# Kernel tuning notes

Measured on AMD Instinct MI355X. Metric: run time of the kernel, lower is better.

## Reference

```python
import jax, jax.numpy as jnp
import numpy as np

N = 50000        # nodes
E = 800000       # edges
FEAT = 64        # cfg.feature_dim
HID = 128        # cfg.hidden_dim
G = 8            # num graphs
EPS = 1e-5       # LayerNorm eps
MIN_DEPTH, MAX_DEPTH = 0.1, 3.0


def _ln(x, g, b):
    m = jnp.mean(x, axis=-1, keepdims=True)
    v = jnp.mean((x - m) ** 2, axis=-1, keepdims=True)
    return (x - m) * jax.lax.rsqrt(v + EPS) * g + b


def setup_inputs() -> dict:
    key = jax.random.key(0)
    ks = jax.random.split(key, 32)
    f32 = jnp.float32
    inp = {}
    inp['x'] = jax.random.normal(ks[0], (N, FEAT), dtype=f32)
    inp['edge_index'] = jax.random.randint(ks[1], (2, E), 0, N)
    inp['batch'] = jnp.sort(jax.random.randint(ks[2], (N,), 0, G))
    # input_projection: Linear(FEAT,HID) + LayerNorm
    inp['in_w'] = jax.random.normal(ks[3], (FEAT, HID), dtype=f32) * (1.0 / np.sqrt(FEAT))
    inp['in_b'] = jnp.zeros((HID,), f32)
    inp['in_ln_g'] = jnp.ones((HID,), f32)
    inp['in_ln_b'] = jnp.zeros((HID,), f32)
    # epigenetics
    inp['methylation'] = jnp.zeros((HID,), f32)
    inp['histones'] = jnp.zeros((4,), f32)
    inp['log_depth'] = jnp.zeros((), f32)
    # NeuralODEFunc: 3 stacked GCNConv(HID,HID) + LayerNorms, gate MLP, residual scalar
    inp['gcn_w'] = jax.random.normal(ks[4], (3, HID, HID), dtype=f32) * (1.0 / np.sqrt(HID))
    inp['gcn_b'] = jnp.zeros((3, HID), f32)
    inp['ln_g'] = jnp.ones((3, HID), f32)
    inp['ln_b'] = jnp.zeros((3, HID), f32)
    inp['gate_w'] = jax.random.normal(ks[5], (2 * HID, HID), dtype=f32) * (1.0 / np.sqrt(2 * HID))
    inp['gate_b'] = jnp.zeros((HID,), f32)
    inp['residual_weight'] = jnp.asarray(0.1, f32)
    # output_projection: Linear(HID,HID) + LayerNorm
    inp['out_w'] = jax.random.normal(ks[6], (HID, HID), dtype=f32) * (1.0 / np.sqrt(HID))
    inp['out_b'] = jnp.zeros((HID,), f32)
    inp['out_ln_g'] = jnp.ones((HID,), f32)
    inp['out_ln_b'] = jnp.zeros((HID,), f32)
    return inp


def reference(x, edge_index, batch, in_w, in_b, in_ln_g, in_ln_b, methylation,
              histones, log_depth, gcn_w, gcn_b, ln_g, ln_b, gate_w, gate_b,
              residual_weight, out_w, out_b, out_ln_g, out_ln_b):
    n = x.shape[0]
    src, dst = edge_index[0], edge_index[1]

    # input_projection (Dropout is identity in eval)
    h = jax.nn.relu(_ln(x @ in_w + in_b, in_ln_g, in_ln_b))

    # epigenetic regulation (chromatin_accessibility goes through .item() -> constant)
    meth_sil = jnp.mean(jax.nn.sigmoid(methylation))
    hm = jax.nn.sigmoid(histones)
    act = (hm[0] + hm[2]) * 0.5
    rep = (hm[1] + hm[3]) * 0.5
    chrom = jax.lax.stop_gradient(jnp.clip(act - rep + 0.5, 0.0, 1.0))
    h = h * (chrom * (1.0 - meth_sil))

    # symmetric GCN normalization, no self loops (computed once, no grad path)
    deg = jax.ops.segment_sum(jnp.ones((E,), h.dtype), dst, num_segments=n)
    dinv = jnp.where(deg > 0, jax.lax.rsqrt(jnp.maximum(deg, 1.0)), 0.0)
    enorm = (dinv[src] * dinv[dst])[:, None]  # [E,1]

    def gcn(hh, i):
        xw = hh @ gcn_w[i]                                   # [N,H]
        agg = jax.ops.segment_sum(xw[src] * enorm, dst, num_segments=n)
        return agg + gcn_b[i]

    def ode_f(hh):
        h_orig = hh
        cur = hh
        for i in range(3):  # fixed layer count
            h_new = _ln(gcn(cur, i), ln_g[i], ln_b[i])
            if i > 0:
                gate = jax.nn.sigmoid(
                    jnp.concatenate([cur, h_new], axis=-1) @ gate_w + gate_b)
                cur = gate * h_new + (1.0 - gate) * cur
            else:
                cur = h_new
        cur = jnp.tanh(cur)
        return cur + residual_weight * h_orig

    # depth via .item() in torch -> non-differentiable constant
    depth = jax.lax.stop_gradient(
        jnp.clip(jnp.exp(log_depth), MIN_DEPTH, MAX_DEPTH))
    # single fixed RK4 step over t = linspace(0, depth, 2)
    dt = depth
    k1 = ode_f(h)
    k2 = ode_f(h + 0.5 * dt * k1)
    k3 = ode_f(h + 0.5 * dt * k2)
    k4 = ode_f(h + dt * k3)
    h_final = h + (dt / 6.0) * (k1 + 2.0 * k2 + 2.0 * k3 + k4)

    # output_projection + global_mean_pool over batch
    h_out = _ln(h_final @ out_w + out_b, out_ln_g, out_ln_b)
    cnt = jax.ops.segment_sum(jnp.ones((n,), h.dtype), batch, num_segments=G)
    pooled = jax.ops.segment_sum(h_out, batch, num_segments=G)
    return pooled / jnp.maximum(cnt, 1.0)[:, None]
```

## Files before the change

### kernel.cpp

```cpp
#include <hip/hip_runtime.h>
#include <math.h>

#define NN 50000
#define EE 800000
#define HH 128
#define FF 64
#define GG 8
#define PB 500
#define SB 1600

using short8 = __attribute__((ext_vector_type(8))) short;
using f32x4  = __attribute__((ext_vector_type(4))) float;
using f32x2  = __attribute__((ext_vector_type(2))) float;

__device__ __forceinline__ float sigm(float x){ return 1.0f/(1.0f+expf(-x)); }
__device__ __forceinline__ unsigned short f2bf(float f){
    union { float f; unsigned u; } v; v.f = f;
    unsigned r = v.u + 0x7fff + ((v.u >> 16) & 1);
    return (unsigned short)(r >> 16);
}
__device__ __forceinline__ float bf2f(unsigned short h){
    union { unsigned u; float f; } v; v.u = ((unsigned)h) << 16;
    return v.f;
}

#if __has_builtin(__builtin_amdgcn_cvt_pk_fp8_f32) && __has_builtin(__builtin_amdgcn_cvt_pk_f32_fp8)
#define FP8_HW 1
#else
#define FP8_HW 0
#endif

__device__ __forceinline__ unsigned fp8enc1_sw(float f){
    union { float fl; unsigned u; } x; x.fl = f;
    unsigned s = (x.u >> 31) << 7;
    float a = fabsf(f);
    if (!(a > 0.f)) return s;
    if (a >= 448.f) return s | 0x7E;
    if (a < 0.015625f) {
        int q = (int)(a * 512.f + 0.5f);
        if (q > 7) return s | (1u << 3);
        return s | (unsigned)q;
    }
    unsigned u = x.u + (1u << 19);
    int e32 = (int)((u >> 23) & 255) - 127;
    if (e32 < -6) { int q=(int)(a*512.f+0.5f); if(q>7)q=7; return s|(unsigned)q; }
    if (e32 > 8) return s | 0x7E;
    unsigned m = (u >> 20) & 7;
    return s | ((unsigned)(e32 + 7) << 3) | m;
}
__device__ __forceinline__ float fp8dec1_sw(unsigned v){
    unsigned s = v >> 7, e = (v >> 3) & 15, m = v & 7;
    float f;
    if (e == 0) f = (float)m * 0.001953125f;
    else { union { unsigned u; float fl; } x; x.u = ((e + 120u) << 23) | (m << 20); f = x.fl; }
    return s ? -f : f;
}
__device__ __forceinline__ unsigned char e2fp8(float a){
#if FP8_HW
    return (unsigned char)(__builtin_amdgcn_cvt_pk_fp8_f32(a, a, 0, false) & 0xFF);
#else
    return (unsigned char)fp8enc1_sw(a);
#endif
}
__device__ __forceinline__ unsigned pk4fp8(float a, float b, float c, float d){
#if FP8_HW
    unsigned p0 = (unsigned)__builtin_amdgcn_cvt_pk_fp8_f32(a, b, 0, false);
    unsigned p1 = (unsigned)__builtin_amdgcn_cvt_pk_fp8_f32(c, d, 0, false);
    return (p0 & 0xFFFFu) | ((p1 & 0xFFFFu) << 16);
#else
    return fp8enc1_sw(a) | (fp8enc1_sw(b) << 8) | (fp8enc1_sw(c) << 16) | (fp8enc1_sw(d) << 24);
#endif
}
__device__ __forceinline__ float2 d2fp8(unsigned short u){
#if FP8_HW
    f32x2 r = __builtin_amdgcn_cvt_pk_f32_fp8((int)(unsigned)u, false);
    return make_float2(r[0], r[1]);
#else
    return make_float2(fp8dec1_sw(u & 0xFF), fp8dec1_sw((u >> 8) & 0xFF));
#endif
}

__global__ void k_setup(const float* __restrict__ meth,
                        const float* __restrict__ histones,
                        const float* __restrict__ logd,
                        float* __restrict__ scal,
                        const int* __restrict__ batch, int* __restrict__ st)
{
    if (blockIdx.x == 1) {
        int g = threadIdx.x;
        if (g > GG) return;
        int lo = 0, hi = NN;
        while (lo < hi) { int mid = (lo + hi) >> 1; if (batch[mid] < g) lo = mid + 1; else hi = mid; }
        st[g] = lo;
        return;
    }
    int l = threadIdx.x;
    float s = sigm(meth[l]) + sigm(meth[l + 64]);
#pragma unroll
    for (int o = 32; o >= 1; o >>= 1) s += __shfl_xor(s, o, 64);
    if (l == 0) {
        float msil = s * (1.0f / 128.0f);
        float h0 = sigm(histones[0]), h1 = sigm(histones[1]);
        float h2 = sigm(histones[2]), h3 = sigm(histones[3]);
        float act = (h0 + h2) * 0.5f, rep = (h1 + h3) * 0.5f;
        float chrom = fminf(fmaxf(act - rep + 0.5f, 0.0f), 1.0f);
        scal[0] = chrom * (1.0f - msil);
        float d = expf(logd[0]);
        scal[1] = fminf(fmaxf(d, 0.1f), 3.0f);
    }
}

__global__ void k_packall(const float* __restrict__ in_w, const float* __restrict__ gcn_w,
                          const float* __restrict__ gate_w, const float* __restrict__ out_w,
                          unsigned short* __restrict__ outp)
{
    int i = blockIdx.x * 256 + threadIdx.x;
    if (i >= 8192 + 6 * 16384) return;
    const float* src; int base, li;
    if (i < 8192) { src = in_w + i; base = 0; li = i; }
    else {
        int j = i - 8192;
        int m = j >> 14, r = j & 16383;
        base = 8192 + (m << 14); li = r;
        if (m < 3)      src = gcn_w  + m * 16384 + r;
        else if (m < 5) src = gate_w + (m - 3) * 16384 + r;
        else            src = out_w + r;
    }
    int k = li >> 7, n = li & 127;
    int c = k >> 5, kl = k & 31, q = kl >> 3, j2 = kl & 7;
    int b = n >> 4, ln = n & 15;
    int lane = q * 16 + ln;
    outp[base + ((c * 8 + b) * 64 + lane) * 8 + j2] = f2bf(*src);
}

__global__ void k_cvtx(const float* __restrict__ x, unsigned short* __restrict__ xb)
{
    size_t i = (size_t)blockIdx.x * 256 + threadIdx.x;
    if (i >= (size_t)NN * 16) return;
    float4 v = ((const float4*)x)[i];
    ushort4 o;
    o.x = f2bf(v.x); o.y = f2bf(v.y); o.z = f2bf(v.z); o.w = f2bf(v.w);
    ((ushort4*)xb)[i] = o;
}

__global__ void k_hist(const int* __restrict__ ei, int* __restrict__ hist)
{
    int e = blockIdx.x * 256 + threadIdx.x;
    if (e < EE) atomicAdd(&hist[ei[EE + e]], 1);
}

__global__ void k_dinv(const int* __restrict__ hist, float* __restrict__ dinv)
{
    int n = blockIdx.x * 256 + threadIdx.x;
    if (n < NN) {
        int d = hist[n];
        dinv[n] = d > 0 ? rsqrtf((float)d) : 0.0f;
    }
}

__global__ void k_scan_a(const int* __restrict__ hist, int* __restrict__ aux)
{
    __shared__ int sh[256];
    int b = blockIdx.x, t = threadIdx.x;
    int base = b * 1024 + t * 4;
    int s = 0;
#pragma unroll
    for (int j = 0; j < 4; ++j) { int i = base + j; if (i < NN) s += hist[i]; }
    sh[t] = s; __syncthreads();
    for (int o = 128; o >= 1; o >>= 1) { if (t < o) sh[t] += sh[t + o]; __syncthreads(); }
    if (t == 0) aux[b] = sh[0];
}

__global__ void k_scan_b(int* __restrict__ aux, int nb)
{
    if (blockIdx.x == 0 && threadIdx.x == 0) {
        int run = 0;
        for (int i = 0; i < nb; ++i) { int v = aux[i]; aux[i] = run; run += v; }
    }
}

__global__ void k_scan_c(const int* __restrict__ hist, const int* __restrict__ aux,
                         int* __restrict__ row_ptr)
{
    __shared__ int sh[256];
    int b = blockIdx.x, t = threadIdx.x;
    int base = b * 1024 + t * 4;
    int v[4]; int s = 0;
#pragma unroll
    for (int j = 0; j < 4; ++j) { int i = base + j; v[j] = (i < NN) ? hist[i] : 0; s += v[j]; }
    sh[t] = s; __syncthreads();
    for (int o = 1; o < 256; o <<= 1) {
        int x = 0; if (t >= o) x = sh[t - o];
        __syncthreads(); sh[t] += x; __syncthreads();
    }
    int run = aux[b] + sh[t] - s;
#pragma unroll
    for (int j = 0; j < 4; ++j) { int i = base + j; if (i < NN) row_ptr[i] = run; run += v[j]; }
    if (b == 0 && t == 0) row_ptr[NN] = EE;
}

__global__ __launch_bounds__(256) void k_scatter(const int* __restrict__ ei,
                          const float* __restrict__ dinv,
                          int* __restrict__ cursor, uint2* __restrict__ ew)
{
    if (blockIdx.x == 0 && threadIdx.x < 128)
        ew[EE + threadIdx.x] = make_uint2(0u, 0u);
    const int grp = blockIdx.x & 7;
    const int blk = blockIdx.x >> 3;
    const int CH  = EE / (SB / 8);
    const int e0 = blk * CH, e1 = e0 + CH;
    const int glo = grp * (NN / 8), ghi = glo + (NN / 8);
    for (int e = e0 + threadIdx.x; e < e1; e += 256) {
        int d = ei[EE + e];
        if (d >= glo && d < ghi) {
            int s = ei[e];
            int p = atomicAdd(&cursor[d], 1);
            ew[p] = make_uint2((unsigned)(s & 0xFFFF) | ((unsigned)(d & 15) << 16),
                               __float_as_uint(dinv[s] * dinv[d]));
        }
    }
}

template<int KC, int MODE>
__global__ __launch_bounds__(256) void k_dense_mfma(
    const unsigned short* __restrict__ A, const unsigned short* __restrict__ Wp,
    const float* __restrict__ bias, const float* __restrict__ lng,
    const float* __restrict__ lnb, const float* __restrict__ scal,
    unsigned short* __restrict__ out, unsigned char* __restrict__ out8)
{
    __shared__ unsigned short Ws[KC * 4096];
    const int t = threadIdx.x;
    {
        const float4* src = (const float4*)Wp;
        float4* dst = (float4*)Ws;
#pragma unroll
        for (int i = 0; i < KC * 2; ++i) dst[t + i * 256] = src[t + i * 256];
    }
    __syncthreads();
    const int wave = t >> 6, lane = t & 63;
    const int quad = lane >> 4, ln = lane & 15;
    const int r0 = blockIdx.x * 64 + wave * 16;
    const int K = KC * 32;
    const int arow = r0 + ln;
    const bool av = arow < NN;

    f32x4 acc[8] = {};
#pragma unroll
    for (int c = 0; c < KC; ++c) {
        short8 a = {};
        if (av) a = *(const short8*)(A + (size_t)arow * K + c * 32 + quad * 8);
#pragma unroll
        for (int b = 0; b < 8; ++b) {
            short8 bb = *(const short8*)&Ws[((c * 8 + b) * 64 + lane) * 8];
            acc[b] = __builtin_amdgcn_mfma_f32_16x16x32_bf16(a, bb, acc[b], 0, 0, 0);
        }
    }

    float b_s[8], g_s[8], e_s[8];
#pragma unroll
    for (int b = 0; b < 8; ++b) {
        int col = b * 16 + ln;
        b_s[b] = bias[col]; g_s[b] = lng[col]; e_s[b] = lnb[col];
    }
    float sc = (MODE == 1) ? scal[0] : 0.0f;
#pragma unroll
    for (int i = 0; i < 4; ++i) {
        int row = r0 + quad * 4 + i;
        float v[8]; float s = 0.f, q = 0.f;
#pragma unroll
        for (int b = 0; b < 8; ++b) { float x = acc[b][i] + b_s[b]; v[b] = x; s += x; q += x * x; }
#pragma unroll
        for (int o = 1; o < 16; o <<= 1) { s += __shfl_xor(s, o, 64); q += __shfl_xor(q, o, 64); }
        float m  = s * (1.0f / 128.0f);
        float vr = q * (1.0f / 128.0f) - m * m;
        float rs = rsqrtf(vr + 1e-5f);
        if (row < NN) {
#pragma unroll
            for (int b = 0; b < 8; ++b) {
                float o2 = (v[b] - m) * rs * g_s[b] + e_s[b];
                if (MODE == 1) o2 = fmaxf(o2, 0.f) * sc;
                out[(size_t)row * 128 + b * 16 + ln] = f2bf(o2);
                if (out8) out8[(size_t)row * 128 + b * 16 + ln] = e2fp8(o2);
            }
        }
    }
}

__global__ __launch_bounds__(128) void k_spgemm(
    const int* __restrict__ rp, const uint2* __restrict__ ew,
    const unsigned char* __restrict__ X8, const unsigned short* __restrict__ Wp,
    const float* __restrict__ bias, const float* __restrict__ lng,
    const float* __restrict__ lnb, unsigned short* __restrict__ out,
    unsigned char* __restrict__ out8)
{
    __shared__ float accf[2][16 * 132];
    const int t = threadIdx.x, wave = t >> 6, lane = t & 63;
    const int quad = lane >> 4, ln = lane & 15;
    const int half = lane >> 5, li = lane & 31;
    const int n0 = blockIdx.x * 16;
    const int nf = n0 + wave * 8;

    {
        float* z0 = &accf[0][wave * 8 * 132];
        float* z1 = &accf[1][wave * 8 * 132];
        for (int i = lane; i < 8 * 132; i += 64) { z0[i] = 0.f; z1[i] = 0.f; }
    }

    if (nf < NN) {
        const int nl = min(nf + 8, NN);
        const int ebeg = __builtin_amdgcn_readfirstlane(rp[nf]);
        const int eend = __builtin_amdgcn_readfirstlane(rp[nl]);
        if (ebeg < eend) {
            float4 racc = make_float4(0.f, 0.f, 0.f, 0.f);
            int curd = (int)((ew[min(ebeg + half, eend - 1)].x >> 16) & 15u);
            const unsigned char* Xl = X8 + li * 4;
            uint2 rec[8], recN[8]; unsigned g[8];
#pragma unroll
            for (int j = 0; j < 8; ++j) rec[j]  = ew[ebeg + 2 * j + half];
#pragma unroll
            for (int j = 0; j < 8; ++j) recN[j] = ew[ebeg + 16 + 2 * j + half];
#pragma unroll
            for (int j = 0; j < 8; ++j) {
                int src = (int)(rec[j].x & 0xFFFFu);
                g[j] = *(const unsigned*)(Xl + (size_t)src * 128);
            }
            for (int e = ebeg; e < eend; e += 16) {
                unsigned gN[8]; uint2 recNN[8];
#pragma unroll
                for (int j = 0; j < 8; ++j) {
                    int src = (int)(recN[j].x & 0xFFFFu);
                    gN[j] = *(const unsigned*)(Xl + (size_t)src * 128);
                }
#pragma unroll
                for (int j = 0; j < 8; ++j) recNN[j] = ew[e + 32 + 2 * j + half];
                int lim = eend - e;
                int mj = lim > half ? ((lim - half + 1) >> 1) : 0; if (mj > 8) mj = 8;
#pragma unroll
                for (int j = 0; j < 8; ++j) {
                    if (j >= mj) break;
                    float wgt = __uint_as_float(rec[j].y);
                    int dl = (int)((rec[j].x >> 16) & 15u);
                    if (dl != curd) {
                        *(float4*)&accf[half][curd * 132 + li * 4] = racc;
                        racc = make_float4(0.f, 0.f, 0.f, 0.f);
                        curd = dl;
                    }
                    float2 p0 = d2fp8((unsigned short)(g[j] & 0xFFFFu));
                    float2 p1 = d2fp8((unsigned short)(g[j] >> 16));
                    racc.x = fmaf(wgt, p0.x, racc.x);
                    racc.y = fmaf(wgt, p0.y, racc.y);
                    racc.z = fmaf(wgt, p1.x, racc.z);
                    racc.w = fmaf(wgt, p1.y, racc.w);
                }
#pragma unroll
                for (int j = 0; j < 8; ++j) { rec[j] = recN[j]; recN[j] = recNN[j]; g[j] = gN[j]; }
            }
            *(float4*)&accf[half][curd * 132 + li * 4] = racc;
        }
    }
    __syncthreads();

    f32x4 acc[8] = {};
    const float* ar0 = &accf[0][(size_t)ln * 132];
    const float* ar1 = &accf[1][(size_t)ln * 132];
#pragma unroll
    for (int c = 0; c < 4; ++c) {
        float4 a0 = *(const float4*)(ar0 + c * 32 + quad * 8);
        float4 a1 = *(const float4*)(ar0 + c * 32 + quad * 8 + 4);
        float4 b0 = *(const float4*)(ar1 + c * 32 + quad * 8);
        float4 b1 = *(const float4*)(ar1 + c * 32 + quad * 8 + 4);
        short8 af;
        af[0] = (short)f2bf(a0.x + b0.x); af[1] = (short)f2bf(a0.y + b0.y);
        af[2] = (short)f2bf(a0.z + b0.z); af[3] = (short)f2bf(a0.w + b0.w);
        af[4] = (short)f2bf(a1.x + b1.x); af[5] = (short)f2bf(a1.y + b1.y);
        af[6] = (short)f2bf(a1.z + b1.z); af[7] = (short)f2bf(a1.w + b1.w);
#pragma unroll
        for (int b = 0; b < 8; ++b) {
            short8 bb = *(const short8*)(Wp + ((size_t)(c * 8 + b) * 64 + lane) * 8);
            acc[b] = __builtin_amdgcn_mfma_f32_16x16x32_bf16(af, bb, acc[b], 0, 0, 0);
        }
    }

    float b_s[8], g_s[8], e_s[8];
#pragma unroll
    for (int b = 0; b < 8; ++b) {
        int col = b * 16 + ln;
        b_s[b] = bias[col]; g_s[b] = lng[col]; e_s[b] = lnb[col];
    }
#pragma unroll
    for (int i = 0; i < 4; ++i) {
        int row = n0 + quad * 4 + i;
        float v[8]; float s = 0.f, q = 0.f;
#pragma unroll
        for (int b = 0; b < 8; ++b) { float x = acc[b][i] + b_s[b]; v[b] = x; s += x; q += x * x; }
#pragma unroll
        for (int o = 1; o < 16; o <<= 1) { s += __shfl_xor(s, o, 64); q += __shfl_xor(q, o, 64); }
        float m  = s * (1.0f / 128.0f);
        float vr = q * (1.0f / 128.0f) - m * m;
        float rs = rsqrtf(vr + 1e-5f);
        if (((quad >> 1) == wave) && row < NN) {
#pragma unroll
            for (int b = 0; b < 8; ++b) {
                float o2 = (v[b] - m) * rs * g_s[b] + e_s[b];
                out[(size_t)row * 128 + b * 16 + ln] = f2bf(o2);
                if (out8) out8[(size_t)row * 128 + b * 16 + ln] = e2fp8(o2);
            }
        }
    }
}

__global__ __launch_bounds__(256) void k_gate_mfma(
    unsigned short* __restrict__ cur, const unsigned short* __restrict__ hnew,
    const unsigned short* __restrict__ Wp, const float* __restrict__ gb,
    unsigned char* __restrict__ cur8)
{
    __shared__ unsigned short Ws[16384];
    const int t = threadIdx.x;
    const int wave = t >> 6, lane = t & 63;
    const int quad = lane >> 4, ln = lane & 15;
    const int r0 = blockIdx.x * 64 + wave * 16;
    const int arow = r0 + ln;
    const bool av = arow < NN;

    f32x4 acc[8] = {};
#pragma unroll
    for (int s = 0; s < 2; ++s) {
        __syncthreads();
        {
            const float4* src = (const float4*)(Wp + (size_t)s * 16384);
            float4* dst = (float4*)Ws;
#pragma unroll
            for (int i = 0; i < 8; ++i) dst[t + i * 256] = src[t + i * 256];
        }
        __syncthreads();
        const unsigned short* A = s ? hnew : cur;
#pragma unroll
        for (int c = 0; c < 4; ++c) {
            short8 a = {};
            if (av) a = *(const short8*)(A + (size_t)arow * 128 + c * 32 + quad * 8);
#pragma unroll
            for (int b = 0; b < 8; ++b) {
                short8 bb = *(const short8*)&Ws[((c * 8 + b) * 64 + lane) * 8];
                acc[b] = __builtin_amdgcn_mfma_f32_16x16x32_bf16(a, bb, acc[b], 0, 0, 0);
            }
        }
    }

    float gb_s[8];
#pragma unroll
    for (int b = 0; b < 8; ++b) gb_s[b] = gb[b * 16 + ln];
#pragma unroll
    for (int i = 0; i < 4; ++i) {
        int row = r0 + quad * 4 + i;
        if (row < NN) {
#pragma unroll
            for (int b = 0; b < 8; ++b) {
                size_t idx = (size_t)row * 128 + b * 16 + ln;
                float g  = sigm(acc[b][i] + gb_s[b]);
                float cu = bf2f(cur[idx]);
                float hn = bf2f(hnew[idx]);
                float r  = g * hn + (1.f - g) * cu;
                cur[idx]  = f2bf(r);
                cur8[idx] = e2fp8(r);
            }
        }
    }
}

template<int S>
__global__ __launch_bounds__(256) void k_stage(
    const unsigned short* __restrict__ cur, const unsigned short* __restrict__ fin,
    const unsigned short* __restrict__ h0, float* __restrict__ acc,
    unsigned short* __restrict__ ybuf, const float* __restrict__ scal,
    const float* __restrict__ rwp, unsigned char* __restrict__ y8)
{
    size_t i = (size_t)blockIdx.x * 256 + threadIdx.x;
    if (i >= (size_t)NN * 32) return;
    float dt = scal[1], rw = rwp[0];
    float wk = (S == 1 || S == 4) ? dt * (1.f / 6.f) : dt * (1.f / 3.f);
    ushort4 c4 = ((const ushort4*)cur)[i];
    ushort4 f4 = ((const ushort4*)fin)[i];
    ushort4 h4 = ((const ushort4*)h0)[i];
    float tv[4];
    tv[0] = tanhf(bf2f(c4.x)) + rw * bf2f(f4.x);
    tv[1] = tanhf(bf2f(c4.y)) + rw * bf2f(f4.y);
    tv[2] = tanhf(bf2f(c4.z)) + rw * bf2f(f4.z);
    tv[3] = tanhf(bf2f(c4.w)) + rw * bf2f(f4.w);
    float4 a;
    if (S == 1) { a.x = wk*tv[0]; a.y = wk*tv[1]; a.z = wk*tv[2]; a.w = wk*tv[3]; }
    else {
        a = ((const float4*)acc)[i];
        a.x += wk*tv[0]; a.y += wk*tv[1]; a.z += wk*tv[2]; a.w += wk*tv[3];
    }
    ((float4*)acc)[i] = a;
    float h[4] = { bf2f(h4.x), bf2f(h4.y), bf2f(h4.z), bf2f(h4.w) };
    float yv[4];
    if (S == 4) {
        yv[0] = h[0] + a.x; yv[1] = h[1] + a.y; yv[2] = h[2] + a.z; yv[3] = h[3] + a.w;
    } else {
        float cn = (S == 3) ? dt : 0.5f * dt;
        yv[0] = h[0] + cn*tv[0]; yv[1] = h[1] + cn*tv[1];
        yv[2] = h[2] + cn*tv[2]; yv[3] = h[3] + cn*tv[3];
    }
    ushort4 y;
    y.x = f2bf(yv[0]); y.y = f2bf(yv[1]); y.z = f2bf(yv[2]); y.w = f2bf(yv[3]);
    ((ushort4*)ybuf)[i] = y;
    ((unsigned*)y8)[i] = pk4fp8(yv[0], yv[1], yv[2], yv[3]);
}

__global__ __launch_bounds__(128) void k_pool1(
    const unsigned short* __restrict__ h, const int* __restrict__ batch,
    float* __restrict__ partial)
{
    int c = threadIdx.x, b = blockIdx.x;
    int r0 = b * (NN / PB), r1 = r0 + (NN / PB);
    float acc = 0.f;
    int gfirst = batch[r0], g = gfirst;
#pragma unroll 4
    for (int r = r0; r < r1; ++r) {
        int gg = batch[r];
        if (gg != g) {
            partial[(size_t)b * 1024 + g * 128 + c] = acc;
            for (int z = g + 1; z < gg; ++z) partial[(size_t)b * 1024 + z * 128 + c] = 0.f;
            acc = 0.f; g = gg;
        }
        acc += bf2f(h[(size_t)r * 128 + c]);
    }
    partial[(size_t)b * 1024 + g * 128 + c] = acc;
    for (int z = 0; z < gfirst; ++z)  partial[(size_t)b * 1024 + z * 128 + c] = 0.f;
    for (int z = g + 1; z < GG; ++z)  partial[(size_t)b * 1024 + z * 128 + c] = 0.f;
}

__global__ __launch_bounds__(256) void k_pool2(
    const float* __restrict__ partial, const int* __restrict__ st,
    float* __restrict__ out)
{
    __shared__ float sh[8][32];
    int cb = blockIdx.x & 3, g = blockIdx.x >> 2;
    int cl = threadIdx.x & 31, sl = threadIdx.x >> 5;
    int c = cb * 32 + cl;
    float s = 0.f;
    for (int b = sl; b < PB; b += 8) s += partial[(size_t)b * 1024 + g * 128 + c];
    sh[sl][cl] = s; __syncthreads();
    if (sl == 0) {
        float tt = 0.f;
#pragma unroll
        for (int i = 0; i < 8; ++i) tt += sh[i][cl];
        int cnt = st[g + 1] - st[g];
        out[g * 128 + c] = tt / (float)(cnt > 0 ? cnt : 1);
    }
}

static inline size_t al(size_t x) { return (x + 255) & ~(size_t)255; }

extern "C" void kernel_launch(void* const* d_in, const int* in_sizes, int n_in,
                              void* d_out, int out_size, void* d_ws, size_t ws_size,
                              hipStream_t stream)
{
    const float* x       = (const float*)d_in[0];
    const int*   ei      = (const int*)d_in[1];
    const int*   batch   = (const int*)d_in[2];
    const float* in_w    = (const float*)d_in[3];
    const float* in_b    = (const float*)d_in[4];
    const float* in_lng  = (const float*)d_in[5];
    const float* in_lnb  = (const float*)d_in[6];
    const float* meth    = (const float*)d_in[7];
    const float* histn   = (const float*)d_in[8];
    const float* logd    = (const float*)d_in[9];
    const float* gcn_w   = (const float*)d_in[10];
    const float* gcn_b   = (const float*)d_in[11];
    const float* ln_g    = (const float*)d_in[12];
    const float* ln_b    = (const float*)d_in[13];
    const float* gate_w  = (const float*)d_in[14];
    const float* gate_b  = (const float*)d_in[15];
    const float* rw      = (const float*)d_in[16];
    const float* out_w   = (const float*)d_in[17];
    const float* out_b   = (const float*)d_in[18];
    const float* out_lng = (const float*)d_in[19];
    const float* out_lnb = (const float*)d_in[20];
    float* out = (float*)d_out;

    char* w = (char*)d_ws;
    size_t off = 0;
    float* scal   = (float*)(w + off); off += al(16 * 4);
    int*   hist   = (int*)(w + off);   off += al((size_t)NN * 4);
    int*   rp     = (int*)(w + off);   off += al((size_t)(NN + 1) * 4);
    int*   cursor = (int*)(w + off);   off += al((size_t)(NN + 1) * 4);
    int*   aux    = (int*)(w + off);   off += al(64 * 4);
    int*   st     = (int*)(w + off);   off += al(16 * 4);
    float* dinv   = (float*)(w + off); off += al((size_t)NN * 4);
    uint2* ew     = (uint2*)(w + off); off += al((size_t)(EE + 128) * 8);
    float* partial= (float*)(w + off); off += al((size_t)PB * 1024 * 4);
    unsigned short* wpak = (unsigned short*)(w + off); off += al((size_t)(8192 + 6 * 16384) * 2);
    unsigned short* inwp  = wpak;
    unsigned short* gcnwp = wpak + 8192;
    unsigned short* gwp   = wpak + 8192 + 3 * 16384;
    unsigned short* owp   = wpak + 8192 + 5 * 16384;
    size_t B16 = al((size_t)NN * 128 * 2);
    unsigned short* xb  = (unsigned short*)(w + off); off += al((size_t)NN * 64 * 2);
    unsigned short* h0  = (unsigned short*)(w + off); off += B16;
    unsigned short* y   = (unsigned short*)(w + off); off += B16;
    unsigned short* cur = (unsigned short*)(w + off); off += B16;
    unsigned short* t2  = (unsigned short*)(w + off); off += B16;
    float* acc = (float*)(w + off); off += al((size_t)NN * 128 * 4);
    size_t B8 = al((size_t)NN * 128);
    unsigned char* h08  = (unsigned char*)(w + off); off += B8;
    unsigned char* y8   = (unsigned char*)(w + off); off += B8;
    unsigned char* cur8 = (unsigned char*)(w + off); off += B8;
    if (off > ws_size) return;

    hipMemsetAsync(hist, 0, (size_t)NN * 4, stream);

    k_setup<<<2, 64, 0, stream>>>(meth, histn, logd, scal, batch, st);
    k_packall<<<(8192 + 6 * 16384 + 255) / 256, 256, 0, stream>>>(in_w, gcn_w, gate_w, out_w, wpak);
    k_cvtx<<<3125, 256, 0, stream>>>(x, xb);

    k_hist<<<(EE + 255) / 256, 256, 0, stream>>>(ei, hist);
    k_dinv<<<(NN + 255) / 256, 256, 0, stream>>>(hist, dinv);
    k_scan_a<<<49, 256, 0, stream>>>(hist, aux);
    k_scan_b<<<1, 1, 0, stream>>>(aux, 49);
    k_scan_c<<<49, 256, 0, stream>>>(hist, aux, rp);
    hipMemcpyAsync(cursor, rp, (size_t)(NN + 1) * 4, hipMemcpyDeviceToDevice, stream);
    k_scatter<<<SB, 256, 0, stream>>>(ei, dinv, cursor, ew);

    const int DG = (NN + 63) / 64;
    const int SG = (NN + 15) / 16;
    k_dense_mfma<2, 1><<<DG, 256, 0, stream>>>(xb, inwp, in_b, in_lng, in_lnb, scal, h0, h08);

    for (int s = 1; s <= 4; ++s) {
        const unsigned short* fin = (s == 1) ? h0 : y;
        const unsigned char*  fin8 = (s == 1) ? h08 : y8;
        k_spgemm<<<SG, 128, 0, stream>>>(rp, ew, fin8, gcnwp, gcn_b, ln_g, ln_b, cur, cur8);
        for (int i = 1; i <= 2; ++i) {
            k_spgemm<<<SG, 128, 0, stream>>>(rp, ew, cur8,
                                             gcnwp + (size_t)i * 128 * 128, gcn_b + i * 128,
                                             ln_g + i * 128, ln_b + i * 128, t2, (unsigned char*)0);
            k_gate_mfma<<<DG, 256, 0, stream>>>(cur, t2, gwp, gate_b, cur8);
        }
        if (s == 1)      k_stage<1><<<6250, 256, 0, stream>>>(cur, fin, h0, acc, y, scal, rw, y8);
        else if (s == 2) k_stage<2><<<6250, 256, 0, stream>>>(cur, fin, h0, acc, y, scal, rw, y8);
        else if (s == 3) k_stage<3><<<6250, 256, 0, stream>>>(cur, fin, h0, acc, y, scal, rw, y8);
        else             k_stage<4><<<6250, 256, 0, stream>>>(cur, fin, h0, acc, y, scal, rw, y8);
    }

    k_dense_mfma<4, 0><<<DG, 256, 0, stream>>>(y, owp, out_b, out_lng, out_lnb, scal, t2, (unsigned char*)0);
    k_pool1<<<PB, 128, 0, stream>>>(t2, batch, partial);
    k_pool2<<<GG * 4, 256, 0, stream>>>(partial, st, out);
}
```

Measured before the change: 893.6 us.

## Fuse last gate with RK4 stage update and use single LDS accumulator in SpMM

The final gate kernel of each ODE evaluation now also applies tanh, the residual, the RK4 accumulation and the next-stage input write, which removes the separate stage kernel and its extra round trip through global memory. In the sparse aggregation kernel, the two per-half LDS accumulators become one buffer updated with LDS atomic adds, which halves shared memory so an occupancy hint of 8 blocks per CU can be declared. The cost is atomic contention on LDS flushes and per-element scalar global accesses in the fused epilogue. The fused gate kernel also skips writing cur/cur8, since nothing downstream reads them.

```diff
diff --git a/kernel.cpp b/kernel.cpp
--- a/kernel.cpp
+++ b/kernel.cpp
@@ -286,14 +286,14 @@
     }
 }
 
-__global__ __launch_bounds__(128) void k_spgemm(
+__global__ __launch_bounds__(128, 8) void k_spgemm(
     const int* __restrict__ rp, const uint2* __restrict__ ew,
     const unsigned char* __restrict__ X8, const unsigned short* __restrict__ Wp,
     const float* __restrict__ bias, const float* __restrict__ lng,
     const float* __restrict__ lnb, unsigned short* __restrict__ out,
     unsigned char* __restrict__ out8)
 {
-    __shared__ float accf[2][16 * 132];
+    __shared__ float accf[16 * 132];
     const int t = threadIdx.x, wave = t >> 6, lane = t & 63;
     const int quad = lane >> 4, ln = lane & 15;
     const int half = lane >> 5, li = lane & 31;
@@ -301,9 +301,8 @@
     const int nf = n0 + wave * 8;
 
     {
-        float* z0 = &accf[0][wave * 8 * 132];
-        float* z1 = &accf[1][wave * 8 * 132];
-        for (int i = lane; i < 8 * 132; i += 64) { z0[i] = 0.f; z1[i] = 0.f; }
+        float* z = &accf[wave * 8 * 132];
+        for (int i = lane; i < 8 * 132; i += 64) z[i] = 0.f;
     }
 
     if (nf < NN) {
@@ -341,7 +340,11 @@
                     float wgt = __uint_as_float(rec[j].y);
                     int dl = (int)((rec[j].x >> 16) & 15u);
                     if (dl != curd) {
-                        *(float4*)&accf[half][curd * 132 + li * 4] = racc;
+                        float* p = &accf[curd * 132 + li * 4];
+                        atomicAdd(p + 0, racc.x);
+                        atomicAdd(p + 1, racc.y);
+                        atomicAdd(p + 2, racc.z);
+                        atomicAdd(p + 3, racc.w);
                         racc = make_float4(0.f, 0.f, 0.f, 0.f);
                         curd = dl;
                     }
@@ -355,25 +358,28 @@
 #pragma unroll
                 for (int j = 0; j < 8; ++j) { rec[j] = recN[j]; recN[j] = recNN[j]; g[j] = gN[j]; }
             }
-            *(float4*)&accf[half][curd * 132 + li * 4] = racc;
+            {
+                float* p = &accf[curd * 132 + li * 4];
+                atomicAdd(p + 0, racc.x);
+                atomicAdd(p + 1, racc.y);
+                atomicAdd(p + 2, racc.z);
+                atomicAdd(p + 3, racc.w);
+            }
         }
     }
     __syncthreads();
 
     f32x4 acc[8] = {};
-    const float* ar0 = &accf[0][(size_t)ln * 132];
-    const float* ar1 = &accf[1][(size_t)ln * 132];
+    const float* ar0 = &accf[(size_t)ln * 132];
 #pragma unroll
     for (int c = 0; c < 4; ++c) {
         float4 a0 = *(const float4*)(ar0 + c * 32 + quad * 8);
         float4 a1 = *(const float4*)(ar0 + c * 32 + quad * 8 + 4);
-        float4 b0 = *(const float4*)(ar1 + c * 32 + quad * 8);
-        float4 b1 = *(const float4*)(ar1 + c * 32 + quad * 8 + 4);
         short8 af;
-        af[0] = (short)f2bf(a0.x + b0.x); af[1] = (short)f2bf(a0.y + b0.y);
-        af[2] = (short)f2bf(a0.z + b0.z); af[3] = (short)f2bf(a0.w + b0.w);
-        af[4] = (short)f2bf(a1.x + b1.x); af[5] = (short)f2bf(a1.y + b1.y);
-        af[6] = (short)f2bf(a1.z + b1.z); af[7] = (short)f2bf(a1.w + b1.w);
+        af[0] = (short)f2bf(a0.x); af[1] = (short)f2bf(a0.y);
+        af[2] = (short)f2bf(a0.z); af[3] = (short)f2bf(a0.w);
+        af[4] = (short)f2bf(a1.x); af[5] = (short)f2bf(a1.y);
+        af[6] = (short)f2bf(a1.z); af[7] = (short)f2bf(a1.w);
 #pragma unroll
         for (int b = 0; b < 8; ++b) {
             short8 bb = *(const short8*)(Wp + ((size_t)(c * 8 + b) * 64 + lane) * 8);
@@ -468,44 +474,73 @@
 }
 
 template<int S>
-__global__ __launch_bounds__(256) void k_stage(
-    const unsigned short* __restrict__ cur, const unsigned short* __restrict__ fin,
-    const unsigned short* __restrict__ h0, float* __restrict__ acc,
-    unsigned short* __restrict__ ybuf, const float* __restrict__ scal,
-    const float* __restrict__ rwp, unsigned char* __restrict__ y8)
-{
-    size_t i = (size_t)blockIdx.x * 256 + threadIdx.x;
-    if (i >= (size_t)NN * 32) return;
-    float dt = scal[1], rw = rwp[0];
-    float wk = (S == 1 || S == 4) ? dt * (1.f / 6.f) : dt * (1.f / 3.f);
-    ushort4 c4 = ((const ushort4*)cur)[i];
-    ushort4 f4 = ((const ushort4*)fin)[i];
-    ushort4 h4 = ((const ushort4*)h0)[i];
-    float tv[4];
-    tv[0] = tanhf(bf2f(c4.x)) + rw * bf2f(f4.x);
-    tv[1] = tanhf(bf2f(c4.y)) + rw * bf2f(f4.y);
-    tv[2] = tanhf(bf2f(c4.z)) + rw * bf2f(f4.z);
-    tv[3] = tanhf(bf2f(c4.w)) + rw * bf2f(f4.w);
-    float4 a;
-    if (S == 1) { a.x = wk*tv[0]; a.y = wk*tv[1]; a.z = wk*tv[2]; a.w = wk*tv[3]; }
-    else {
-        a = ((const float4*)acc)[i];
-        a.x += wk*tv[0]; a.y += wk*tv[1]; a.z += wk*tv[2]; a.w += wk*tv[3];
-    }
-    ((float4*)acc)[i] = a;
-    float h[4] = { bf2f(h4.x), bf2f(h4.y), bf2f(h4.z), bf2f(h4.w) };
-    float yv[4];
-    if (S == 4) {
-        yv[0] = h[0] + a.x; yv[1] = h[1] + a.y; yv[2] = h[2] + a.z; yv[3] = h[3] + a.w;
-    } else {
-        float cn = (S == 3) ? dt : 0.5f * dt;
-        yv[0] = h[0] + cn*tv[0]; yv[1] = h[1] + cn*tv[1];
-        yv[2] = h[2] + cn*tv[2]; yv[3] = h[3] + cn*tv[3];
-    }
-    ushort4 y;
-    y.x = f2bf(yv[0]); y.y = f2bf(yv[1]); y.z = f2bf(yv[2]); y.w = f2bf(yv[3]);
-    ((ushort4*)ybuf)[i] = y;
-    ((unsigned*)y8)[i] = pk4fp8(yv[0], yv[1], yv[2], yv[3]);
+__global__ __launch_bounds__(256) void k_gate_fused(
+    const unsigned short* __restrict__ cur, const unsigned short* __restrict__ hnew,
+    const unsigned short* __restrict__ Wp, const float* __restrict__ gb,
+    const unsigned short* __restrict__ fin, const unsigned short* __restrict__ h0,
+    float* __restrict__ acc, unsigned short* __restrict__ ybuf,
+    unsigned char* __restrict__ y8, const float* __restrict__ scal,
+    const float* __restrict__ rwp)
+{
+    __shared__ unsigned short Ws[16384];
+    const int t = threadIdx.x;
+    const int wave = t >> 6, lane = t & 63;
+    const int quad = lane >> 4, ln = lane & 15;
+    const int r0 = blockIdx.x * 64 + wave * 16;
+    const int arow = r0 + ln;
+    const bool av = arow < NN;
+
+    f32x4 am[8] = {};
+#pragma unroll
+    for (int s = 0; s < 2; ++s) {
+        __syncthreads();
+        {
+            const float4* src = (const float4*)(Wp + (size_t)s * 16384);
+            float4* dst = (float4*)Ws;
+#pragma unroll
+            for (int i = 0; i < 8; ++i) dst[t + i * 256] = src[t + i * 256];
+        }
+        __syncthreads();
+        const unsigned short* A = s ? hnew : cur;
+#pragma unroll
+        for (int c = 0; c < 4; ++c) {
+            short8 a = {};
+            if (av) a = *(const short8*)(A + (size_t)arow * 128 + c * 32 + quad * 8);
+#pragma unroll
+            for (int b = 0; b < 8; ++b) {
+                short8 bb = *(const short8*)&Ws[((c * 8 + b) * 64 + lane) * 8];
+                am[b] = __builtin_amdgcn_mfma_f32_16x16x32_bf16(a, bb, am[b], 0, 0, 0);
+            }
+        }
+    }
+
+    float gb_s[8];
+#pragma unroll
+    for (int b = 0; b < 8; ++b) gb_s[b] = gb[b * 16 + ln];
+    const float dt = scal[1], rw = rwp[0];
+    const float wk = (S == 1 || S == 4) ? dt * (1.f / 6.f) : dt * (1.f / 3.f);
+    const float cn = (S == 3) ? dt : 0.5f * dt;
+#pragma unroll
+    for (int i = 0; i < 4; ++i) {
+        int row = r0 + quad * 4 + i;
+        if (row < NN) {
+#pragma unroll
+            for (int b = 0; b < 8; ++b) {
+                size_t idx = (size_t)row * 128 + b * 16 + ln;
+                float g  = sigm(am[b][i] + gb_s[b]);
+                float cu = bf2f(cur[idx]);
+                float hn = bf2f(hnew[idx]);
+                float r  = g * hn + (1.f - g) * cu;
+                float tv = tanhf(r) + rw * bf2f(fin[idx]);
+                float a  = (S == 1) ? wk * tv : acc[idx] + wk * tv;
+                acc[idx] = a;
+                float yv = (S == 4) ? bf2f(h0[idx]) + a
+                                    : bf2f(h0[idx]) + cn * tv;
+                ybuf[idx] = f2bf(yv);
+                y8[idx]   = e2fp8(yv);
+            }
+        }
+    }
 }
 
 __global__ __launch_bounds__(128) void k_pool1(
@@ -631,16 +666,17 @@
         const unsigned short* fin = (s == 1) ? h0 : y;
         const unsigned char*  fin8 = (s == 1) ? h08 : y8;
         k_spgemm<<<SG, 128, 0, stream>>>(rp, ew, fin8, gcnwp, gcn_b, ln_g, ln_b, cur, cur8);
-        for (int i = 1; i <= 2; ++i) {
-            k_spgemm<<<SG, 128, 0, stream>>>(rp, ew, cur8,
-                                             gcnwp + (size_t)i * 128 * 128, gcn_b + i * 128,
-                                             ln_g + i * 128, ln_b + i * 128, t2, (unsigned char*)0);
-            k_gate_mfma<<<DG, 256, 0, stream>>>(cur, t2, gwp, gate_b, cur8);
-        }
-        if (s == 1)      k_stage<1><<<6250, 256, 0, stream>>>(cur, fin, h0, acc, y, scal, rw, y8);
-        else if (s == 2) k_stage<2><<<6250, 256, 0, stream>>>(cur, fin, h0, acc, y, scal, rw, y8);
-        else if (s == 3) k_stage<3><<<6250, 256, 0, stream>>>(cur, fin, h0, acc, y, scal, rw, y8);
-        else             k_stage<4><<<6250, 256, 0, stream>>>(cur, fin, h0, acc, y, scal, rw, y8);
+        k_spgemm<<<SG, 128, 0, stream>>>(rp, ew, cur8,
+                                         gcnwp + (size_t)1 * 128 * 128, gcn_b + 128,
+                                         ln_g + 128, ln_b + 128, t2, (unsigned char*)0);
+        k_gate_mfma<<<DG, 256, 0, stream>>>(cur, t2, gwp, gate_b, cur8);
+        k_spgemm<<<SG, 128, 0, stream>>>(rp, ew, cur8,
+                                         gcnwp + (size_t)2 * 128 * 128, gcn_b + 256,
+                                         ln_g + 256, ln_b + 256, t2, (unsigned char*)0);
+        if (s == 1)      k_gate_fused<1><<<DG, 256, 0, stream>>>(cur, t2, gwp, gate_b, fin, h0, acc, y, y8, scal, rw);
+        else if (s == 2) k_gate_fused<2><<<DG, 256, 0, stream>>>(cur, t2, gwp, gate_b, fin, h0, acc, y, y8, scal, rw);
+        else if (s == 3) k_gate_fused<3><<<DG, 256, 0, stream>>>(cur, t2, gwp, gate_b, fin, h0, acc, y, y8, scal, rw);
+        else             k_gate_fused<4><<<DG, 256, 0, stream>>>(cur, t2, gwp, gate_b, fin, h0, acc, y, y8, scal, rw);
     }
 
     k_dense_mfma<4, 0><<<DG, 256, 0, stream>>>(y, owp, out_b, out_lng, out_lnb, scal, t2, (unsigned char*)0);
```

New measurement: 2.177 ms. 2.44x slower.
